# Kernel optimization log

Hardware: AMD Instinct MI355X
Metric: run time of the kernel (lower is better)

The kernel has to match this reference:

```python
import jax, jax.numpy as jnp
import numpy as np

EPS = 1e-5


def _layernorm(x, w, b):
    mu = jnp.mean(x, axis=-1, keepdims=True)
    var = jnp.var(x, axis=-1, keepdims=True)
    return (x - mu) * jax.lax.rsqrt(var + EPS) * w + b


def setup_inputs() -> dict:
    key = jax.random.key(0)
    ks = jax.random.split(key, 5)
    B, I, H = 8192, 1024, 1024
    inp = {
        "input": jax.random.normal(ks[0], (B, I), dtype=jnp.float32),
        "hx": jax.random.normal(ks[1], (B, H), dtype=jnp.float32),
        "cx": jax.random.normal(ks[2], (B, H), dtype=jnp.float32),
        # parameters (torch initializes weights with randn; LN weight=1, bias=0)
        "weight_ih": jax.random.normal(ks[3], (4 * H, I), dtype=jnp.float32),
        "weight_hh": jax.random.normal(ks[4], (4 * H, H), dtype=jnp.float32),
        "ln_i_w": jnp.ones((4 * H,), jnp.float32),
        "ln_i_b": jnp.zeros((4 * H,), jnp.float32),
        "ln_h_w": jnp.ones((4 * H,), jnp.float32),
        "ln_h_b": jnp.zeros((4 * H,), jnp.float32),
        "ln_c_w": jnp.ones((H,), jnp.float32),
        "ln_c_b": jnp.zeros((H,), jnp.float32),
    }
    return inp


def reference(input, hx, cx, weight_ih, weight_hh,
              ln_i_w, ln_i_b, ln_h_w, ln_h_b, ln_c_w, ln_c_b):
    # gate pre-activations: [B, 4H]
    igates = _layernorm(input @ weight_ih.T, ln_i_w, ln_i_b)
    hgates = _layernorm(hx @ weight_hh.T, ln_h_w, ln_h_b)
    gates = igates + hgates
    ingate, forgetgate, cellgate, outgate = jnp.split(gates, 4, axis=-1)
    ingate = jax.nn.sigmoid(ingate)
    forgetgate = jax.nn.sigmoid(forgetgate)
    cellgate = jnp.tanh(cellgate)
    outgate = jax.nn.sigmoid(outgate)
    cy = _layernorm(forgetgate * cx + ingate * cellgate, ln_c_w, ln_c_b)
    hy = outgate * jnp.tanh(cy)  # activation=Tanh, dropout p=0 is identity
    return (hy, cy)
```

## Files before the change

### kernel.cpp

```cpp
#include <hip/hip_runtime.h>
#include <hip/hip_bf16.h>
#include <cstdint>
#include <cstddef>

typedef __bf16 bf16_t;
typedef bf16_t bf16x8 __attribute__((ext_vector_type(8)));
typedef bf16_t bf16x4v __attribute__((ext_vector_type(4)));
typedef float floatx4 __attribute__((ext_vector_type(4)));

static constexpr int B_ = 8192;
static constexpr int H_ = 1024;
static constexpr int G4 = 4096;
static constexpr int K_ = 1024;

__device__ inline void async_copy16(const bf16_t* g, bf16_t* l) {
  auto l3 = (__attribute__((address_space(3))) void*)(uint32_t)(uintptr_t)l;
  __builtin_amdgcn_global_load_lds(
      (__attribute__((address_space(1))) void*)(uintptr_t)g, l3, 16, 0, 0);
}

__global__ __launch_bounds__(256) void cast2_f32_bf16(
    const float* __restrict__ a, const float* __restrict__ b,
    bf16_t* __restrict__ oa, bf16_t* __restrict__ ob, int n8each) {
  int gid = blockIdx.x * blockDim.x + threadIdx.x;
  const float* src; bf16_t* dst; int idx;
  if (gid < n8each) { src = a; dst = oa; idx = gid; }
  else              { src = b; dst = ob; idx = gid - n8each; }
  const float4 v0 = ((const float4*)src)[idx * 2];
  const float4 v1 = ((const float4*)src)[idx * 2 + 1];
  bf16x8 o;
  o[0] = (bf16_t)v0.x; o[1] = (bf16_t)v0.y; o[2] = (bf16_t)v0.z; o[3] = (bf16_t)v0.w;
  o[4] = (bf16_t)v1.x; o[5] = (bf16_t)v1.y; o[6] = (bf16_t)v1.z; o[7] = (bf16_t)v1.w;
  ((bf16x8*)dst)[idx] = o;
}

__global__ __launch_bounds__(256) void cast_w_perm(
    const float* __restrict__ wih, const float* __restrict__ whh,
    bf16_t* __restrict__ oih, bf16_t* __restrict__ ohh) {
  const int rp = blockIdx.x & 4095;
  const float* src = (blockIdx.x < 4096) ? wih : whh;
  bf16_t*      dst = (blockIdx.x < 4096) ? oih : ohh;
  const int h = rp >> 2, g = rp & 3;
  const int rin = g * 1024 + h;
  const int c = threadIdx.x * 4;
  const float4 v = *(const float4*)(src + (size_t)rin * K_ + c);
  bf16x4v o;
  o[0] = (bf16_t)v.x; o[1] = (bf16_t)v.y; o[2] = (bf16_t)v.z; o[3] = (bf16_t)v.w;
  *(bf16x4v*)(dst + (size_t)rp * K_ + c) = o;
}

__global__ __launch_bounds__(256) void gemm_bt_dual(
    const bf16_t* __restrict__ A0, const bf16_t* __restrict__ A1,
    const bf16_t* __restrict__ W0, const bf16_t* __restrict__ W1,
    bf16_t* __restrict__ C0, bf16_t* __restrict__ C1) {
  constexpr int N = G4, K = K_;
  const bf16_t* A = blockIdx.z ? A1 : A0;
  const bf16_t* W = blockIdx.z ? W1 : W0;
  bf16_t*       C = blockIdx.z ? C1 : C0;

  __shared__ bf16_t As[128 * 32];
  __shared__ bf16_t Bs[128 * 32];

  const int tid  = threadIdx.x;
  const int lane = tid & 63;
  const int wid  = tid >> 6;
  const int wm   = wid >> 1, wn = wid & 1;
  const int lrow = lane & 15, quad = lane >> 4;

  const int m0 = blockIdx.y * 128;
  const int n0 = blockIdx.x * 128;

  const int L0 = tid;
  const int L1 = 256 + tid;
  const int c0 = (((L0 & 3) ^ ((L0 >> 3) & 3))) * 8;
  const int c1 = (((L1 & 3) ^ ((L1 >> 3) & 3))) * 8;
  const bf16_t* gA0 = A + (size_t)(m0 + (L0 >> 2)) * K + c0;
  const bf16_t* gA1 = A + (size_t)(m0 + (L1 >> 2)) * K + c1;
  const bf16_t* gB0 = W + (size_t)(n0 + (L0 >> 2)) * K + c0;
  const bf16_t* gB1 = W + (size_t)(n0 + (L1 >> 2)) * K + c1;
  bf16_t* lA0 = As + wid * 512;
  bf16_t* lA1 = As + 2048 + wid * 512;
  bf16_t* lB0 = Bs + wid * 512;
  bf16_t* lB1 = Bs + 2048 + wid * 512;

  const int qc = (quad ^ ((lrow >> 1) & 3)) * 8;

  floatx4 acc[4][4] = {};

  for (int k0 = 0; k0 < K; k0 += 32) {
    __syncthreads();
    async_copy16(gA0 + k0, lA0);
    async_copy16(gA1 + k0, lA1);
    async_copy16(gB0 + k0, lB0);
    async_copy16(gB1 + k0, lB1);
    __syncthreads();

    bf16x8 af[4], bfr[4];
#pragma unroll
    for (int i = 0; i < 4; ++i)
      af[i] = *(const bf16x8*)&As[(wm * 64 + i * 16 + lrow) * 32 + qc];
#pragma unroll
    for (int j = 0; j < 4; ++j)
      bfr[j] = *(const bf16x8*)&Bs[(wn * 64 + j * 16 + lrow) * 32 + qc];
#pragma unroll
    for (int i = 0; i < 4; ++i)
#pragma unroll
      for (int j = 0; j < 4; ++j)
        acc[i][j] = __builtin_amdgcn_mfma_f32_16x16x32_bf16(af[i], bfr[j],
                                                            acc[i][j], 0, 0, 0);
  }

#pragma unroll
  for (int i = 0; i < 4; ++i) {
    const int mbase = m0 + wm * 64 + i * 16 + quad * 4;
#pragma unroll
    for (int j = 0; j < 4; ++j) {
      const int n = n0 + wn * 64 + j * 16 + lrow;
#pragma unroll
      for (int r = 0; r < 4; ++r)
        C[(size_t)(mbase + r) * N + n] = (bf16_t)acc[i][j][r];
    }
  }
}

__device__ inline float sigmoid_f(float x) { return 1.0f / (1.0f + __expf(-x)); }
__device__ inline float tanh_f(float x) {
  float e = __expf(2.0f * x);
  return 1.0f - 2.0f / (e + 1.0f);
}

__global__ __launch_bounds__(256) void ln_lstm_epilogue(
    const bf16_t* __restrict__ IG, const bf16_t* __restrict__ HG,
    const float* __restrict__ cx,
    const float* __restrict__ wi, const float* __restrict__ bi,
    const float* __restrict__ wh, const float* __restrict__ bh,
    const float* __restrict__ wc, const float* __restrict__ bc,
    float* __restrict__ hy_out, float* __restrict__ cy_out) {
  const int b = blockIdx.x;
  const int t = threadIdx.x;
  const int lane = t & 63;
  const int wid = t >> 6;

  __shared__ float red1[4][4];
  __shared__ float red2[4][2];

  const bf16x8 ig0 = *(const bf16x8*)(IG + (size_t)b * 4096 + t * 16);
  const bf16x8 ig1 = *(const bf16x8*)(IG + (size_t)b * 4096 + t * 16 + 8);
  const bf16x8 hg0 = *(const bf16x8*)(HG + (size_t)b * 4096 + t * 16);
  const bf16x8 hg1 = *(const bf16x8*)(HG + (size_t)b * 4096 + t * 16 + 8);
  const float4 cx4 = *(const float4*)(cx + (size_t)b * 1024 + t * 4);

  float vi[16], vh[16];
#pragma unroll
  for (int e = 0; e < 8; ++e) {
    vi[e] = (float)ig0[e]; vi[8 + e] = (float)ig1[e];
    vh[e] = (float)hg0[e]; vh[8 + e] = (float)hg1[e];
  }
  float si = 0, qi = 0, sh = 0, qh = 0;
#pragma unroll
  for (int k = 0; k < 16; ++k) {
    si += vi[k]; qi = fmaf(vi[k], vi[k], qi);
    sh += vh[k]; qh = fmaf(vh[k], vh[k], qh);
  }
#pragma unroll
  for (int off = 32; off; off >>= 1) {
    si += __shfl_down(si, off); qi += __shfl_down(qi, off);
    sh += __shfl_down(sh, off); qh += __shfl_down(qh, off);
  }
  if (lane == 0) { red1[wid][0] = si; red1[wid][1] = qi; red1[wid][2] = sh; red1[wid][3] = qh; }
  __syncthreads();
  si = red1[0][0] + red1[1][0] + red1[2][0] + red1[3][0];
  qi = red1[0][1] + red1[1][1] + red1[2][1] + red1[3][1];
  sh = red1[0][2] + red1[1][2] + red1[2][2] + red1[3][2];
  qh = red1[0][3] + red1[1][3] + red1[2][3] + red1[3][3];

  const float invN = 1.0f / 4096.0f;
  const float mui = si * invN, muh = sh * invN;
  const float rsi = rsqrtf(fmaxf(qi * invN - mui * mui, 0.0f) + 1e-5f);
  const float rsh = rsqrtf(fmaxf(qh * invN - muh * muh, 0.0f) + 1e-5f);

  float4 wig[4], big[4], whg[4], bhg[4];
#pragma unroll
  for (int g = 0; g < 4; ++g) {
    wig[g] = *(const float4*)(wi + g * 1024 + t * 4);
    big[g] = *(const float4*)(bi + g * 1024 + t * 4);
    whg[g] = *(const float4*)(wh + g * 1024 + t * 4);
    bhg[g] = *(const float4*)(bh + g * 1024 + t * 4);
  }

  const float cxa[4] = {cx4.x, cx4.y, cx4.z, cx4.w};
  float cv[4], ov[4];
  float sc = 0, qc2 = 0;
#pragma unroll
  for (int j = 0; j < 4; ++j) {
    const float wg[4] = {((const float*)&wig[0])[j], ((const float*)&wig[1])[j],
                         ((const float*)&wig[2])[j], ((const float*)&wig[3])[j]};
    const float bg[4] = {((const float*)&big[0])[j], ((const float*)&big[1])[j],
                         ((const float*)&big[2])[j], ((const float*)&big[3])[j]};
    const float wg2[4] = {((const float*)&whg[0])[j], ((const float*)&whg[1])[j],
                          ((const float*)&whg[2])[j], ((const float*)&whg[3])[j]};
    const float bg2[4] = {((const float*)&bhg[0])[j], ((const float*)&bhg[1])[j],
                          ((const float*)&bhg[2])[j], ((const float*)&bhg[3])[j]};
    float G[4];
#pragma unroll
    for (int g = 0; g < 4; ++g) {
      const int e = j * 4 + g;
      G[g] = (vi[e] - mui) * rsi * wg[g] + bg[g] +
             (vh[e] - muh) * rsh * wg2[g] + bg2[g];
    }
    const float in_g = sigmoid_f(G[0]);
    const float fo_g = sigmoid_f(G[1]);
    const float ce_g = tanh_f(G[2]);
    ov[j] = sigmoid_f(G[3]);
    const float c = fo_g * cxa[j] + in_g * ce_g;
    cv[j] = c;
    sc += c; qc2 = fmaf(c, c, qc2);
  }
#pragma unroll
  for (int off = 32; off; off >>= 1) {
    sc += __shfl_down(sc, off); qc2 += __shfl_down(qc2, off);
  }
  if (lane == 0) { red2[wid][0] = sc; red2[wid][1] = qc2; }
  __syncthreads();
  sc = red2[0][0] + red2[1][0] + red2[2][0] + red2[3][0];
  qc2 = red2[0][1] + red2[1][1] + red2[2][1] + red2[3][1];
  const float invH = 1.0f / 1024.0f;
  const float muc = sc * invH;
  const float rsc = rsqrtf(fmaxf(qc2 * invH - muc * muc, 0.0f) + 1e-5f);

  const float4 wc4 = ((const float4*)wc)[t];
  const float4 bc4 = ((const float4*)bc)[t];
  const float wca[4] = {wc4.x, wc4.y, wc4.z, wc4.w};
  const float bca[4] = {bc4.x, bc4.y, bc4.z, bc4.w};
  float4 hyv, cyv;
#pragma unroll
  for (int j = 0; j < 4; ++j) {
    const float cyn = (cv[j] - muc) * rsc * wca[j] + bca[j];
    ((float*)&cyv)[j] = cyn;
    ((float*)&hyv)[j] = ov[j] * tanh_f(cyn);
  }
  *(float4*)(cy_out + (size_t)b * 1024 + t * 4) = cyv;
  *(float4*)(hy_out + (size_t)b * 1024 + t * 4) = hyv;
}

extern "C" void kernel_launch(void* const* d_in, const int* in_sizes, int n_in,
                              void* d_out, int out_size, void* d_ws, size_t ws_size,
                              hipStream_t stream) {
  const float* input  = (const float*)d_in[0];
  const float* hx     = (const float*)d_in[1];
  const float* cx     = (const float*)d_in[2];
  const float* w_ih   = (const float*)d_in[3];
  const float* w_hh   = (const float*)d_in[4];
  const float* ln_i_w = (const float*)d_in[5];
  const float* ln_i_b = (const float*)d_in[6];
  const float* ln_h_w = (const float*)d_in[7];
  const float* ln_h_b = (const float*)d_in[8];
  const float* ln_c_w = (const float*)d_in[9];
  const float* ln_c_b = (const float*)d_in[10];

  float* out = (float*)d_out;
  float* hy = out;
  float* cy = out + (size_t)B_ * H_;

  bf16_t* Abf = (bf16_t*)d_ws;
  bf16_t* Hbf = Abf + (size_t)B_ * K_;
  bf16_t* Wib = Hbf + (size_t)B_ * K_;
  bf16_t* Whb = Wib + (size_t)G4 * K_;
  bf16_t* IG  = Whb + (size_t)G4 * K_;
  bf16_t* HG  = IG + (size_t)B_ * G4;

  const int n8 = B_ * K_ / 8;
  cast2_f32_bf16<<<(2 * n8) / 256, 256, 0, stream>>>(input, hx, Abf, Hbf, n8);
  cast_w_perm<<<2 * G4, 256, 0, stream>>>(w_ih, w_hh, Wib, Whb);

  gemm_bt_dual<<<dim3(G4 / 128, B_ / 128, 2), 256, 0, stream>>>(Abf, Hbf, Wib, Whb, IG, HG);

  ln_lstm_epilogue<<<B_, 256, 0, stream>>>(IG, HG, cx, ln_i_w, ln_i_b,
                                           ln_h_w, ln_h_b, ln_c_w, ln_c_b, hy, cy);
}
```

Before: 379.5 us.

## Double-buffer GEMM LDS with register-staged prefetch and merge cast kernels

New measurement: 772.6 us. 2.04x slower.

```diff
diff --git a/kernel.cpp b/kernel.cpp
--- a/kernel.cpp
+++ b/kernel.cpp
@@ -13,40 +13,40 @@
 static constexpr int G4 = 4096;
 static constexpr int K_ = 1024;
 
-__device__ inline void async_copy16(const bf16_t* g, bf16_t* l) {
-  auto l3 = (__attribute__((address_space(3))) void*)(uint32_t)(uintptr_t)l;
-  __builtin_amdgcn_global_load_lds(
-      (__attribute__((address_space(1))) void*)(uintptr_t)g, l3, 16, 0, 0);
-}
-
-__global__ __launch_bounds__(256) void cast2_f32_bf16(
-    const float* __restrict__ a, const float* __restrict__ b,
-    bf16_t* __restrict__ oa, bf16_t* __restrict__ ob, int n8each) {
-  int gid = blockIdx.x * blockDim.x + threadIdx.x;
-  const float* src; bf16_t* dst; int idx;
-  if (gid < n8each) { src = a; dst = oa; idx = gid; }
-  else              { src = b; dst = ob; idx = gid - n8each; }
-  const float4 v0 = ((const float4*)src)[idx * 2];
-  const float4 v1 = ((const float4*)src)[idx * 2 + 1];
-  bf16x8 o;
-  o[0] = (bf16_t)v0.x; o[1] = (bf16_t)v0.y; o[2] = (bf16_t)v0.z; o[3] = (bf16_t)v0.w;
-  o[4] = (bf16_t)v1.x; o[5] = (bf16_t)v1.y; o[6] = (bf16_t)v1.z; o[7] = (bf16_t)v1.w;
-  ((bf16x8*)dst)[idx] = o;
-}
-
-__global__ __launch_bounds__(256) void cast_w_perm(
+__device__ inline void pipeline_barrier() {
+  __builtin_amdgcn_s_waitcnt(0xC07F);
+  __builtin_amdgcn_s_barrier();
+}
+
+__global__ __launch_bounds__(256) void cast_all(
+    const float* __restrict__ input, const float* __restrict__ hx,
     const float* __restrict__ wih, const float* __restrict__ whh,
-    bf16_t* __restrict__ oih, bf16_t* __restrict__ ohh) {
-  const int rp = blockIdx.x & 4095;
-  const float* src = (blockIdx.x < 4096) ? wih : whh;
-  bf16_t*      dst = (blockIdx.x < 4096) ? oih : ohh;
-  const int h = rp >> 2, g = rp & 3;
-  const int rin = g * 1024 + h;
-  const int c = threadIdx.x * 4;
-  const float4 v = *(const float4*)(src + (size_t)rin * K_ + c);
-  bf16x4v o;
-  o[0] = (bf16_t)v.x; o[1] = (bf16_t)v.y; o[2] = (bf16_t)v.z; o[3] = (bf16_t)v.w;
-  *(bf16x4v*)(dst + (size_t)rp * K_ + c) = o;
+    bf16_t* __restrict__ Abf, bf16_t* __restrict__ Hbf,
+    bf16_t* __restrict__ Wib, bf16_t* __restrict__ Whb) {
+  const int bb = blockIdx.x;
+  const int tid = threadIdx.x;
+  if (bb < 8192) {
+    const float* src = (bb < 4096) ? input : hx;
+    bf16_t* dst      = (bb < 4096) ? Abf : Hbf;
+    const int idx = (bb & 4095) * 256 + tid;
+    const float4 v0 = ((const float4*)src)[idx * 2];
+    const float4 v1 = ((const float4*)src)[idx * 2 + 1];
+    bf16x8 o;
+    o[0] = (bf16_t)v0.x; o[1] = (bf16_t)v0.y; o[2] = (bf16_t)v0.z; o[3] = (bf16_t)v0.w;
+    o[4] = (bf16_t)v1.x; o[5] = (bf16_t)v1.y; o[6] = (bf16_t)v1.z; o[7] = (bf16_t)v1.w;
+    ((bf16x8*)dst)[idx] = o;
+  } else {
+    const int rp = bb & 4095;
+    const float* src = (bb < 12288) ? wih : whh;
+    bf16_t*      dst = (bb < 12288) ? Wib : Whb;
+    const int h = rp >> 2, g = rp & 3;
+    const int rin = g * 1024 + h;
+    const int c = tid * 4;
+    const float4 v = *(const float4*)(src + (size_t)rin * K_ + c);
+    bf16x4v o;
+    o[0] = (bf16_t)v.x; o[1] = (bf16_t)v.y; o[2] = (bf16_t)v.z; o[3] = (bf16_t)v.w;
+    *(bf16x4v*)(dst + (size_t)rp * K_ + c) = o;
+  }
 }
 
 __global__ __launch_bounds__(256) void gemm_bt_dual(
@@ -58,8 +58,8 @@
   const bf16_t* W = blockIdx.z ? W1 : W0;
   bf16_t*       C = blockIdx.z ? C1 : C0;
 
-  __shared__ bf16_t As[128 * 32];
-  __shared__ bf16_t Bs[128 * 32];
+  __shared__ bf16_t As[2][128 * 32];
+  __shared__ bf16_t Bs[2][128 * 32];
 
   const int tid  = threadIdx.x;
   const int lane = tid & 63;
@@ -78,37 +78,75 @@
   const bf16_t* gA1 = A + (size_t)(m0 + (L1 >> 2)) * K + c1;
   const bf16_t* gB0 = W + (size_t)(n0 + (L0 >> 2)) * K + c0;
   const bf16_t* gB1 = W + (size_t)(n0 + (L1 >> 2)) * K + c1;
-  bf16_t* lA0 = As + wid * 512;
-  bf16_t* lA1 = As + 2048 + wid * 512;
-  bf16_t* lB0 = Bs + wid * 512;
-  bf16_t* lB1 = Bs + 2048 + wid * 512;
 
   const int qc = (quad ^ ((lrow >> 1) & 3)) * 8;
 
+  uint4 R0[4], R1[4];
+
+#define GLOAD(R, kofs)                                   \
+  do {                                                   \
+    (R)[0] = *(const uint4*)(gA0 + (kofs));              \
+    (R)[1] = *(const uint4*)(gA1 + (kofs));              \
+    (R)[2] = *(const uint4*)(gB0 + (kofs));              \
+    (R)[3] = *(const uint4*)(gB1 + (kofs));              \
+  } while (0)
+
+#define LDSWRITE(buf, R)                                                  \
+  do {                                                                    \
+    *(uint4*)((char*)&As[buf][0] + tid * 16)        = (R)[0];             \
+    *(uint4*)((char*)&As[buf][0] + 4096 + tid * 16) = (R)[1];             \
+    *(uint4*)((char*)&Bs[buf][0] + tid * 16)        = (R)[2];             \
+    *(uint4*)((char*)&Bs[buf][0] + 4096 + tid * 16) = (R)[3];             \
+  } while (0)
+
   floatx4 acc[4][4] = {};
-
-  for (int k0 = 0; k0 < K; k0 += 32) {
-    __syncthreads();
-    async_copy16(gA0 + k0, lA0);
-    async_copy16(gA1 + k0, lA1);
-    async_copy16(gB0 + k0, lB0);
-    async_copy16(gB1 + k0, lB1);
-    __syncthreads();
-
-    bf16x8 af[4], bfr[4];
-#pragma unroll
-    for (int i = 0; i < 4; ++i)
-      af[i] = *(const bf16x8*)&As[(wm * 64 + i * 16 + lrow) * 32 + qc];
-#pragma unroll
-    for (int j = 0; j < 4; ++j)
-      bfr[j] = *(const bf16x8*)&Bs[(wn * 64 + j * 16 + lrow) * 32 + qc];
-#pragma unroll
-    for (int i = 0; i < 4; ++i)
-#pragma unroll
-      for (int j = 0; j < 4; ++j)
-        acc[i][j] = __builtin_amdgcn_mfma_f32_16x16x32_bf16(af[i], bfr[j],
-                                                            acc[i][j], 0, 0, 0);
-  }
+  bf16x8 af[4], bfr[4];
+
+#define FRAGREAD(buf)                                                          \
+  do {                                                                         \
+    _Pragma("unroll") for (int i = 0; i < 4; ++i)                              \
+        af[i] = *(const bf16x8*)&As[buf][(wm * 64 + i * 16 + lrow) * 32 + qc]; \
+    _Pragma("unroll") for (int j = 0; j < 4; ++j)                              \
+        bfr[j] = *(const bf16x8*)&Bs[buf][(wn * 64 + j * 16 + lrow) * 32 + qc];\
+  } while (0)
+
+#define MFMA16()                                                               \
+  do {                                                                         \
+    _Pragma("unroll") for (int i = 0; i < 4; ++i)                              \
+        _Pragma("unroll") for (int j = 0; j < 4; ++j)                          \
+            acc[i][j] = __builtin_amdgcn_mfma_f32_16x16x32_bf16(               \
+                af[i], bfr[j], acc[i][j], 0, 0, 0);                            \
+  } while (0)
+
+  GLOAD(R0, 0);
+  LDSWRITE(0, R0);
+  GLOAD(R0, 32);
+  pipeline_barrier();
+
+  for (int k2 = 0; k2 < 15; ++k2) {
+    const int kb = k2 * 64;
+    FRAGREAD(0);
+    GLOAD(R1, kb + 64);
+    MFMA16();
+    LDSWRITE(1, R0);
+    pipeline_barrier();
+    FRAGREAD(1);
+    GLOAD(R0, kb + 96);
+    MFMA16();
+    LDSWRITE(0, R1);
+    pipeline_barrier();
+  }
+  FRAGREAD(0);
+  MFMA16();
+  LDSWRITE(1, R0);
+  pipeline_barrier();
+  FRAGREAD(1);
+  MFMA16();
+
+#undef GLOAD
+#undef LDSWRITE
+#undef FRAGREAD
+#undef MFMA16
 
 #pragma unroll
   for (int i = 0; i < 4; ++i) {
@@ -269,9 +307,7 @@
   bf16_t* IG  = Whb + (size_t)G4 * K_;
   bf16_t* HG  = IG + (size_t)B_ * G4;
 
-  const int n8 = B_ * K_ / 8;
-  cast2_f32_bf16<<<(2 * n8) / 256, 256, 0, stream>>>(input, hx, Abf, Hbf, n8);
-  cast_w_perm<<<2 * G4, 256, 0, stream>>>(w_ih, w_hh, Wib, Whb);
+  cast_all<<<16384, 256, 0, stream>>>(input, hx, w_ih, w_hh, Abf, Hbf, Wib, Whb);
 
   gemm_bt_dual<<<dim3(G4 / 128, B_ / 128, 2), 256, 0, stream>>>(Abf, Hbf, Wib, Whb, IG, HG);
 
```
